# Kernel tuning notes

Hardware: AMD Instinct MI355X
Metric: run time of the kernel (lower is better)

The kernel has to match this reference:

```python
import jax, jax.numpy as jnp
import numpy as np

USER_NUM = 100000
ITEM_NUM = 100000
DIM = 64
BS = 256


def setup_inputs() -> dict:
    key = jax.random.key(0)
    k1, k2, k3, k4, k5 = jax.random.split(key, 5)
    # xavier_normal-ish scale for embeddings/linear
    user_table = jax.random.normal(k1, (USER_NUM, DIM), dtype=jnp.float32) * 0.1
    item_table = jax.random.normal(k2, (ITEM_NUM, DIM), dtype=jnp.float32) * 0.1
    cls_w = jax.random.normal(k3, (5, DIM), dtype=jnp.float32) * (2.0 / (DIM + 5)) ** 0.5
    cls_b = jnp.zeros((5,), dtype=jnp.float32)
    batch_user = jax.random.randint(k4, (BS,), 0, USER_NUM, dtype=jnp.int64)
    values = jnp.array([[1.0, 2.0, 3.0, 4.0, 5.0]], dtype=jnp.float32)
    return {
        "batch_user": batch_user,
        "user_table": user_table,
        "item_table": item_table,
        "cls_w": cls_w,
        "cls_b": cls_b,
        "values": values,
    }


def reference(batch_user, user_table, item_table, cls_w, cls_b, values):
    # forward_full_items: score every (user, item) pair.
    # Torch materializes h_ui = (u repeated) * (items tiled) of shape
    # [bs*item_num, dim]; mathematically logits = einsum over dim, so we
    # fuse the broadcasted product with the tiny Linear to avoid the
    # huge expanded intermediate while computing identical math.
    u = user_table[batch_user]                       # [bs, dim]
    # logits[b,i,c] = sum_d u[b,d] * item[i,d] * W[c,d] + b[c]
    logits = jnp.einsum('bd,id,cd->bic', u, item_table, cls_w) + cls_b  # [bs, item_num, 5]
    prob = jax.nn.softmax(logits, axis=-1)
    return jnp.sum(prob * values[0], axis=-1)        # [bs, item_num]
```

## Files before the change

kernel.cpp:

```cpp
#include <hip/hip_runtime.h>

#define I_TOTAL 100000
#define DIM 64
#define BS 256

typedef __attribute__((ext_vector_type(8))) short bf16x8;
typedef __attribute__((ext_vector_type(4))) float f32x4;

__device__ inline unsigned short f2bf(float x) {
    union { float f; unsigned u; } v; v.f = x;
    return (unsigned short)((v.u + 0x8000u) >> 16);
}

__device__ inline unsigned pk_bf16(float lo, float hi) {
    unsigned r;
    asm("v_cvt_pk_bf16_f32 %0, %1, %2" : "=v"(r) : "v"(lo), "v"(hi));
    return r;
}

__device__ inline bf16x8 pack8(float4 a, float4 b) {
    union { unsigned u[4]; bf16x8 v; } r;
    r.u[0] = pk_bf16(a.x, a.y);
    r.u[1] = pk_bf16(a.z, a.w);
    r.u[2] = pk_bf16(b.x, b.y);
    r.u[3] = pk_bf16(b.z, b.w);
    return r.v;
}

__device__ inline float rfl(float x) {
    union { float f; int i; } u; u.f = x;
    u.i = __builtin_amdgcn_readfirstlane(u.i);
    return u.f;
}

__global__ __launch_bounds__(256) void conv_items(
    const float* __restrict__ item, unsigned short* __restrict__ itbf)
{
    long t = (long)blockIdx.x * 256 + threadIdx.x;
    const float4* p = (const float4*)(item + t * 8);
    float4 a = p[0], b = p[1];
    ushort4 r0, r1;
    r0.x = f2bf(a.x); r0.y = f2bf(a.y); r0.z = f2bf(a.z); r0.w = f2bf(a.w);
    r1.x = f2bf(b.x); r1.y = f2bf(b.y); r1.z = f2bf(b.z); r1.w = f2bf(b.w);
    ushort4* q = (ushort4*)(itbf + t * 8);
    q[0] = r0; q[1] = r1;
}

__device__ inline void mfma_tile(const bf16x8 (&afr)[5][2], bf16x8 b0, bf16x8 b1,
                                 f32x4 (&acc)[5])
{
    const f32x4 zero = (f32x4){0.f, 0.f, 0.f, 0.f};
#pragma unroll
    for (int c = 0; c < 5; ++c) {
        acc[c] = __builtin_amdgcn_mfma_f32_16x16x32_bf16(afr[c][0], b0, zero, 0, 0, 0);
        acc[c] = __builtin_amdgcn_mfma_f32_16x16x32_bf16(afr[c][1], b1, acc[c], 0, 0, 0);
    }
}

__device__ inline void softmax_store(const f32x4 (&acc)[5], const float (&sw)[5],
                                     const float (&swv)[5], float* wlds, int ti)
{
#pragma unroll
    for (int rr = 0; rr < 4; ++rr) {
        float e0 = __builtin_amdgcn_exp2f(acc[0][rr]);
        float e1 = __builtin_amdgcn_exp2f(acc[1][rr]);
        float e2 = __builtin_amdgcn_exp2f(acc[2][rr]);
        float e3 = __builtin_amdgcn_exp2f(acc[3][rr]);
        float e4 = __builtin_amdgcn_exp2f(acc[4][rr]);
        float den = e0 * sw[0];
        den = fmaf(e1, sw[1], den);
        den = fmaf(e2, sw[2], den);
        den = fmaf(e3, sw[3], den);
        den = fmaf(e4, sw[4], den);
        float num = e0 * swv[0];
        num = fmaf(e1, swv[1], num);
        num = fmaf(e2, swv[2], num);
        num = fmaf(e3, swv[3], num);
        num = fmaf(e4, swv[4], num);
        wlds[rr * 64 + ti * 16] = num * __builtin_amdgcn_rcpf(den);
    }
}

__global__ __launch_bounds__(256) void gemm_softmax(
    const unsigned short* __restrict__ itbf,
    const int* __restrict__ bu, const float* __restrict__ ut,
    const float* __restrict__ cw, const float* __restrict__ clsb,
    const float* __restrict__ vals, float* __restrict__ out)
{
    __shared__ float ldsb[4224];

    const int blk = blockIdx.x;
    const int r8 = blk & 7;
    const int qq = blk >> 3;
    const int g  = qq & 15;
    const int a  = qq >> 4;
    const int y  = a * 8 + r8;
    if (y >= 98) return;

    const int lane = threadIdx.x & 63;
    const int wave = threadIdx.x >> 6;
    const int col  = lane & 15;
    const int quad = lane >> 4;

    const int b_base = g * 16;
    const int i_base = y * 1024 + wave * 256;

    const float s = 1.4426950408889634f;

    const float* up = ut + (size_t)bu[b_base + col] * DIM + quad * 8;
    float4 u0 = *(const float4*)(up);
    float4 u1 = *(const float4*)(up + 4);
    float4 u2 = *(const float4*)(up + 32);
    float4 u3 = *(const float4*)(up + 36);
    u0.x *= s; u0.y *= s; u0.z *= s; u0.w *= s;
    u1.x *= s; u1.y *= s; u1.z *= s; u1.w *= s;
    u2.x *= s; u2.y *= s; u2.z *= s; u2.w *= s;
    u3.x *= s; u3.y *= s; u3.z *= s; u3.w *= s;

    bf16x8 afr[5][2];
    float sw[5], swv[5];
#pragma unroll
    for (int c = 0; c < 5; ++c) {
        const float* wp = cw + c * DIM + quad * 8;
        float4 w0 = *(const float4*)(wp);
        float4 w1 = *(const float4*)(wp + 4);
        float4 w2 = *(const float4*)(wp + 32);
        float4 w3 = *(const float4*)(wp + 36);
        float4 m0 = make_float4(u0.x*w0.x, u0.y*w0.y, u0.z*w0.z, u0.w*w0.w);
        float4 m1 = make_float4(u1.x*w1.x, u1.y*w1.y, u1.z*w1.z, u1.w*w1.w);
        float4 m2 = make_float4(u2.x*w2.x, u2.y*w2.y, u2.z*w2.z, u2.w*w2.w);
        float4 m3 = make_float4(u3.x*w3.x, u3.y*w3.y, u3.z*w3.z, u3.w*w3.w);
        afr[c][0] = pack8(m0, m1);
        afr[c][1] = pack8(m2, m3);
        float w = __builtin_amdgcn_exp2f(clsb[c] * s);
        sw[c]  = rfl(w);
        swv[c] = rfl(w * vals[c]);
    }

    if (y < 97) {
        float* wlds = ldsb + wave * 1056 + quad * 264 + col;
        const float* rlds = ldsb + wave * 1056 + quad * 264 + 4 * col;

        float* op[4];
#pragma unroll
        for (int k = 0; k < 4; ++k)
            op[k] = out + (size_t)(b_base + quad * 4 + k) * I_TOTAL + (i_base + 4 * col);

        const unsigned short* bp = itbf + (size_t)(i_base + col) * DIM + quad * 8;

        bf16x8 pf0 = *(const bf16x8*)(bp);
        bf16x8 pf1 = *(const bf16x8*)(bp + 32);

        f32x4 accA[5], accB[5];

#pragma unroll 1
        for (int t4 = 0; t4 < 4; ++t4) {
            const unsigned short* base = bp + (size_t)(t4 * 4) * 1024;
            bf16x8 b0, b1;

            b0 = pf0; b1 = pf1;
            pf0 = *(const bf16x8*)(base + 1024);
            pf1 = *(const bf16x8*)(base + 1024 + 32);
            mfma_tile(afr, b0, b1, accA);

            b0 = pf0; b1 = pf1;
            pf0 = *(const bf16x8*)(base + 2048);
            pf1 = *(const bf16x8*)(base + 2048 + 32);
            mfma_tile(afr, b0, b1, accB);
            softmax_store(accA, sw, swv, wlds, 0);

            b0 = pf0; b1 = pf1;
            pf0 = *(const bf16x8*)(base + 3072);
            pf1 = *(const bf16x8*)(base + 3072 + 32);
            mfma_tile(afr, b0, b1, accA);
            softmax_store(accB, sw, swv, wlds, 1);

            b0 = pf0; b1 = pf1;
            pf0 = *(const bf16x8*)(base + 4096);
            pf1 = *(const bf16x8*)(base + 4096 + 32);
            mfma_tile(afr, b0, b1, accB);
            softmax_store(accA, sw, swv, wlds, 2);

            softmax_store(accB, sw, swv, wlds, 3);

#pragma unroll
            for (int k = 0; k < 4; ++k) {
                f32x4 o4 = *(const f32x4*)(rlds + k * 64);
                *(f32x4*)op[k] = o4;
                op[k] += 64;
            }
        }
    } else {
        float vv[5];
#pragma unroll
        for (int c = 0; c < 5; ++c) vv[c] = vals[c];
#pragma unroll 1
        for (int t = 0; t < 16; ++t) {
            int i  = i_base + t * 16 + col;
            int ic = i < I_TOTAL ? i : I_TOTAL - 1;
            const unsigned short* p2 = itbf + (size_t)ic * DIM + quad * 8;
            bf16x8 b0 = *(const bf16x8*)p2;
            bf16x8 b1 = *(const bf16x8*)(p2 + 32);
            f32x4 acc[5];
            mfma_tile(afr, b0, b1, acc);
            if (i < I_TOTAL) {
#pragma unroll
                for (int rr = 0; rr < 4; ++rr) {
                    float e0 = __builtin_amdgcn_exp2f(acc[0][rr]);
                    float e1 = __builtin_amdgcn_exp2f(acc[1][rr]);
                    float e2 = __builtin_amdgcn_exp2f(acc[2][rr]);
                    float e3 = __builtin_amdgcn_exp2f(acc[3][rr]);
                    float e4 = __builtin_amdgcn_exp2f(acc[4][rr]);
                    float den = e0 * sw[0];
                    den = fmaf(e1, sw[1], den);
                    den = fmaf(e2, sw[2], den);
                    den = fmaf(e3, sw[3], den);
                    den = fmaf(e4, sw[4], den);
                    float num = e0 * swv[0];
                    num = fmaf(e1, swv[1], num);
                    num = fmaf(e2, swv[2], num);
                    num = fmaf(e3, swv[3], num);
                    num = fmaf(e4, swv[4], num);
                    out[(size_t)(b_base + quad * 4 + rr) * I_TOTAL + i] =
                        num * __builtin_amdgcn_rcpf(den);
                }
            }
        }
        (void)vv;
    }
}

__global__ __launch_bounds__(256) void gemm_softmax_fb(
    const int* __restrict__ bu, const float* __restrict__ ut,
    const float* __restrict__ it, const float* __restrict__ cw,
    const float* __restrict__ clsb, const float* __restrict__ vals,
    float* __restrict__ out)
{
    __shared__ float ldsb[4224];

    const int blk = blockIdx.x;
    const int r8 = blk & 7;
    const int qq = blk >> 3;
    const int g  = qq & 15;
    const int a  = qq >> 4;
    const int y  = a * 8 + r8;
    if (y >= 98) return;

    const int lane = threadIdx.x & 63;
    const int wave = threadIdx.x >> 6;
    const int col  = lane & 15;
    const int quad = lane >> 4;

    const int b_base = g * 16;
    const int i_base = y * 1024 + wave * 256;

    const float s = 1.4426950408889634f;

    const float* up = ut + (size_t)bu[b_base + col] * DIM + quad * 8;
    float4 u0 = *(const float4*)(up);
    float4 u1 = *(const float4*)(up + 4);
    float4 u2 = *(const float4*)(up + 32);
    float4 u3 = *(const float4*)(up + 36);
    u0.x *= s; u0.y *= s; u0.z *= s; u0.w *= s;
    u1.x *= s; u1.y *= s; u1.z *= s; u1.w *= s;
    u2.x *= s; u2.y *= s; u2.z *= s; u2.w *= s;
    u3.x *= s; u3.y *= s; u3.z *= s; u3.w *= s;

    bf16x8 afr[5][2];
    f32x4 cin[5];
    float vv[5];
#pragma unroll
    for (int c = 0; c < 5; ++c) {
        const float* wp = cw + c * DIM + quad * 8;
        float4 w0 = *(const float4*)(wp);
        float4 w1 = *(const float4*)(wp + 4);
        float4 w2 = *(const float4*)(wp + 32);
        float4 w3 = *(const float4*)(wp + 36);
        float4 m0 = make_float4(u0.x*w0.x, u0.y*w0.y, u0.z*w0.z, u0.w*w0.w);
        float4 m1 = make_float4(u1.x*w1.x, u1.y*w1.y, u1.z*w1.z, u1.w*w1.w);
        float4 m2 = make_float4(u2.x*w2.x, u2.y*w2.y, u2.z*w2.z, u2.w*w2.w);
        float4 m3 = make_float4(u3.x*w3.x, u3.y*w3.y, u3.z*w3.z, u3.w*w3.w);
        afr[c][0] = pack8(m0, m1);
        afr[c][1] = pack8(m2, m3);
        float bc = clsb[c] * s;
        cin[c] = (f32x4){bc, bc, bc, bc};
        vv[c] = vals[c];
    }

    if (y < 97) {
        float* wlds = ldsb + wave * 1056 + quad * 264 + col;
        const float* rlds = ldsb + wave * 1056 + quad * 264 + 4 * col;

        float* op[4];
#pragma unroll
        for (int k = 0; k < 4; ++k)
            op[k] = out + (size_t)(b_base + quad * 4 + k) * I_TOTAL + (i_base + 4 * col);

        const float* bp = it + (size_t)(i_base + col) * DIM + quad * 8;

#pragma unroll 1
        for (int t4 = 0; t4 < 4; ++t4) {
#pragma unroll
            for (int ti = 0; ti < 4; ++ti) {
                const float* p = bp + ti * 1024;
                float4 q0 = *(const float4*)(p);
                float4 q1 = *(const float4*)(p + 4);
                float4 q2 = *(const float4*)(p + 32);
                float4 q3 = *(const float4*)(p + 36);
                bf16x8 b0 = pack8(q0, q1);
                bf16x8 b1 = pack8(q2, q3);
                f32x4 acc[5];
#pragma unroll
                for (int c = 0; c < 5; ++c) {
                    acc[c] = __builtin_amdgcn_mfma_f32_16x16x32_bf16(afr[c][0], b0, cin[c], 0, 0, 0);
                    acc[c] = __builtin_amdgcn_mfma_f32_16x16x32_bf16(afr[c][1], b1, acc[c], 0, 0, 0);
                }
#pragma unroll
                for (int rr = 0; rr < 4; ++rr) {
                    float e0 = __builtin_amdgcn_exp2f(acc[0][rr]);
                    float e1 = __builtin_amdgcn_exp2f(acc[1][rr]);
                    float e2 = __builtin_amdgcn_exp2f(acc[2][rr]);
                    float e3 = __builtin_amdgcn_exp2f(acc[3][rr]);
                    float e4 = __builtin_amdgcn_exp2f(acc[4][rr]);
                    float den = ((e0 + e1) + (e2 + e3)) + e4;
                    float num = e0 * vv[0];
                    num = fmaf(e1, vv[1], num);
                    num = fmaf(e2, vv[2], num);
                    num = fmaf(e3, vv[3], num);
                    num = fmaf(e4, vv[4], num);
                    wlds[rr * 64 + ti * 16] = num * __builtin_amdgcn_rcpf(den);
                }
            }
#pragma unroll
            for (int k = 0; k < 4; ++k) {
                f32x4 o4 = *(const f32x4*)(rlds + k * 64);
                *(f32x4*)op[k] = o4;
                op[k] += 64;
            }
            bp += 4 * 1024;
        }
    } else {
#pragma unroll 1
        for (int t = 0; t < 16; ++t) {
            int i  = i_base + t * 16 + col;
            int ic = i < I_TOTAL ? i : I_TOTAL - 1;
            const float* p2 = it + (size_t)ic * DIM + quad * 8;
            float4 q0 = *(const float4*)(p2);
            float4 q1 = *(const float4*)(p2 + 4);
            float4 q2 = *(const float4*)(p2 + 32);
            float4 q3 = *(const float4*)(p2 + 36);
            bf16x8 b0 = pack8(q0, q1);
            bf16x8 b1 = pack8(q2, q3);
            f32x4 acc[5];
#pragma unroll
            for (int c = 0; c < 5; ++c) {
                acc[c] = __builtin_amdgcn_mfma_f32_16x16x32_bf16(afr[c][0], b0, cin[c], 0, 0, 0);
                acc[c] = __builtin_amdgcn_mfma_f32_16x16x32_bf16(afr[c][1], b1, acc[c], 0, 0, 0);
            }
            if (i < I_TOTAL) {
#pragma unroll
                for (int rr = 0; rr < 4; ++rr) {
                    float e0 = __builtin_amdgcn_exp2f(acc[0][rr]);
                    float e1 = __builtin_amdgcn_exp2f(acc[1][rr]);
                    float e2 = __builtin_amdgcn_exp2f(acc[2][rr]);
                    float e3 = __builtin_amdgcn_exp2f(acc[3][rr]);
                    float e4 = __builtin_amdgcn_exp2f(acc[4][rr]);
                    float den = ((e0 + e1) + (e2 + e3)) + e4;
                    float num = e0 * vv[0];
                    num = fmaf(e1, vv[1], num);
                    num = fmaf(e2, vv[2], num);
                    num = fmaf(e3, vv[3], num);
                    num = fmaf(e4, vv[4], num);
                    out[(size_t)(b_base + quad * 4 + rr) * I_TOTAL + i] =
                        num * __builtin_amdgcn_rcpf(den);
                }
            }
        }
    }
}

extern "C" void kernel_launch(void* const* d_in, const int* in_sizes, int n_in,
                              void* d_out, int out_size, void* d_ws, size_t ws_size,
                              hipStream_t stream) {
    const int*   bu   = (const int*)d_in[0];
    const float* ut   = (const float*)d_in[1];
    const float* it   = (const float*)d_in[2];
    const float* cw   = (const float*)d_in[3];
    const float* cb   = (const float*)d_in[4];
    const float* vals = (const float*)d_in[5];
    float* out = (float*)d_out;
    unsigned short* itbf = (unsigned short*)d_ws;

    const size_t needed = (size_t)I_TOTAL * DIM * 2;

    if (ws_size >= needed) {
        conv_items<<<3125, 256, 0, stream>>>(it, itbf);
        gemm_softmax<<<1664, 256, 0, stream>>>(itbf, bu, ut, cw, cb, vals, out);
    } else {
        gemm_softmax_fb<<<1664, 256, 0, stream>>>(bu, ut, it, cw, cb, vals, out);
    }
}
```

Before: 177.8 us.

## Split fused GEMM-softmax blocks into single-wave workgroups and drop manual prefetch

The main kernel now launches one wave per workgroup (6656 blocks of 64 threads) instead of four waves per block, with the wave index folded into the block index and a smaller LDS buffer per block. The hand-written software prefetch and double accumulator pipeline is replaced by a simple unrolled loop over four tiles, leaving scheduling to the compiler. The fallback kernel is refactored to use the shared mfma_tile/softmax_store helpers with the exp-bias weighting. The smaller blocks aim to improve scheduling granularity and occupancy, but they lose the explicit load/compute overlap.

```diff
diff --git a/kernel.cpp b/kernel.cpp
--- a/kernel.cpp
+++ b/kernel.cpp
@@ -81,29 +81,30 @@
     }
 }
 
-__global__ __launch_bounds__(256) void gemm_softmax(
+__global__ __launch_bounds__(64) void gemm_softmax(
     const unsigned short* __restrict__ itbf,
     const int* __restrict__ bu, const float* __restrict__ ut,
     const float* __restrict__ cw, const float* __restrict__ clsb,
     const float* __restrict__ vals, float* __restrict__ out)
 {
-    __shared__ float ldsb[4224];
-
-    const int blk = blockIdx.x;
-    const int r8 = blk & 7;
-    const int qq = blk >> 3;
-    const int g  = qq & 15;
-    const int a  = qq >> 4;
-    const int y  = a * 8 + r8;
+    __shared__ float ldsb[1056];
+
+    const int blk  = blockIdx.x;
+    const int r8   = blk & 7;
+    const int rest = blk >> 3;
+    const int wv   = rest & 3;
+    const int qq   = rest >> 2;
+    const int g    = qq & 15;
+    const int a    = qq >> 4;
+    const int y    = a * 8 + r8;
     if (y >= 98) return;
 
     const int lane = threadIdx.x & 63;
-    const int wave = threadIdx.x >> 6;
     const int col  = lane & 15;
     const int quad = lane >> 4;
 
     const int b_base = g * 16;
-    const int i_base = y * 1024 + wave * 256;
+    const int i_base = y * 1024 + wv * 256;
 
     const float s = 1.4426950408889634f;
 
@@ -138,8 +139,8 @@
     }
 
     if (y < 97) {
-        float* wlds = ldsb + wave * 1056 + quad * 264 + col;
-        const float* rlds = ldsb + wave * 1056 + quad * 264 + 4 * col;
+        float* wlds = ldsb + quad * 264 + col;
+        const float* rlds = ldsb + quad * 264 + 4 * col;
 
         float* op[4];
 #pragma unroll
@@ -148,52 +149,25 @@
 
         const unsigned short* bp = itbf + (size_t)(i_base + col) * DIM + quad * 8;
 
-        bf16x8 pf0 = *(const bf16x8*)(bp);
-        bf16x8 pf1 = *(const bf16x8*)(bp + 32);
-
-        f32x4 accA[5], accB[5];
-
 #pragma unroll 1
         for (int t4 = 0; t4 < 4; ++t4) {
-            const unsigned short* base = bp + (size_t)(t4 * 4) * 1024;
-            bf16x8 b0, b1;
-
-            b0 = pf0; b1 = pf1;
-            pf0 = *(const bf16x8*)(base + 1024);
-            pf1 = *(const bf16x8*)(base + 1024 + 32);
-            mfma_tile(afr, b0, b1, accA);
-
-            b0 = pf0; b1 = pf1;
-            pf0 = *(const bf16x8*)(base + 2048);
-            pf1 = *(const bf16x8*)(base + 2048 + 32);
-            mfma_tile(afr, b0, b1, accB);
-            softmax_store(accA, sw, swv, wlds, 0);
-
-            b0 = pf0; b1 = pf1;
-            pf0 = *(const bf16x8*)(base + 3072);
-            pf1 = *(const bf16x8*)(base + 3072 + 32);
-            mfma_tile(afr, b0, b1, accA);
-            softmax_store(accB, sw, swv, wlds, 1);
-
-            b0 = pf0; b1 = pf1;
-            pf0 = *(const bf16x8*)(base + 4096);
-            pf1 = *(const bf16x8*)(base + 4096 + 32);
-            mfma_tile(afr, b0, b1, accB);
-            softmax_store(accA, sw, swv, wlds, 2);
-
-            softmax_store(accB, sw, swv, wlds, 3);
-
+#pragma unroll
+            for (int ti = 0; ti < 4; ++ti) {
+                bf16x8 b0 = *(const bf16x8*)(bp + ti * 1024);
+                bf16x8 b1 = *(const bf16x8*)(bp + ti * 1024 + 32);
+                f32x4 acc[5];
+                mfma_tile(afr, b0, b1, acc);
+                softmax_store(acc, sw, swv, wlds, ti);
+            }
 #pragma unroll
             for (int k = 0; k < 4; ++k) {
                 f32x4 o4 = *(const f32x4*)(rlds + k * 64);
                 *(f32x4*)op[k] = o4;
                 op[k] += 64;
             }
+            bp += 4 * 1024;
         }
     } else {
-        float vv[5];
-#pragma unroll
-        for (int c = 0; c < 5; ++c) vv[c] = vals[c];
 #pragma unroll 1
         for (int t = 0; t < 16; ++t) {
             int i  = i_base + t * 16 + col;
@@ -226,7 +200,6 @@
                 }
             }
         }
-        (void)vv;
     }
 }
 
@@ -267,8 +240,7 @@
     u3.x *= s; u3.y *= s; u3.z *= s; u3.w *= s;
 
     bf16x8 afr[5][2];
-    f32x4 cin[5];
-    float vv[5];
+    float sw[5], swv[5];
 #pragma unroll
     for (int c = 0; c < 5; ++c) {
         const float* wp = cw + c * DIM + quad * 8;
@@ -282,9 +254,9 @@
         float4 m3 = make_float4(u3.x*w3.x, u3.y*w3.y, u3.z*w3.z, u3.w*w3.w);
         afr[c][0] = pack8(m0, m1);
         afr[c][1] = pack8(m2, m3);
-        float bc = clsb[c] * s;
-        cin[c] = (f32x4){bc, bc, bc, bc};
-        vv[c] = vals[c];
+        float w = __builtin_amdgcn_exp2f(clsb[c] * s);
+        sw[c]  = rfl(w);
+        swv[c] = rfl(w * vals[c]);
     }
 
     if (y < 97) {
@@ -310,26 +282,8 @@
                 bf16x8 b0 = pack8(q0, q1);
                 bf16x8 b1 = pack8(q2, q3);
                 f32x4 acc[5];
-#pragma unroll
-                for (int c = 0; c < 5; ++c) {
-                    acc[c] = __builtin_amdgcn_mfma_f32_16x16x32_bf16(afr[c][0], b0, cin[c], 0, 0, 0);
-                    acc[c] = __builtin_amdgcn_mfma_f32_16x16x32_bf16(afr[c][1], b1, acc[c], 0, 0, 0);
-                }
-#pragma unroll
-                for (int rr = 0; rr < 4; ++rr) {
-                    float e0 = __builtin_amdgcn_exp2f(acc[0][rr]);
-                    float e1 = __builtin_amdgcn_exp2f(acc[1][rr]);
-                    float e2 = __builtin_amdgcn_exp2f(acc[2][rr]);
-                    float e3 = __builtin_amdgcn_exp2f(acc[3][rr]);
-                    float e4 = __builtin_amdgcn_exp2f(acc[4][rr]);
-                    float den = ((e0 + e1) + (e2 + e3)) + e4;
-                    float num = e0 * vv[0];
-                    num = fmaf(e1, vv[1], num);
-                    num = fmaf(e2, vv[2], num);
-                    num = fmaf(e3, vv[3], num);
-                    num = fmaf(e4, vv[4], num);
-                    wlds[rr * 64 + ti * 16] = num * __builtin_amdgcn_rcpf(den);
-                }
+                mfma_tile(afr, b0, b1, acc);
+                softmax_store(acc, sw, swv, wlds, ti);
             }
 #pragma unroll
             for (int k = 0; k < 4; ++k) {
@@ -352,11 +306,7 @@
             bf16x8 b0 = pack8(q0, q1);
             bf16x8 b1 = pack8(q2, q3);
             f32x4 acc[5];
-#pragma unroll
-            for (int c = 0; c < 5; ++c) {
-                acc[c] = __builtin_amdgcn_mfma_f32_16x16x32_bf16(afr[c][0], b0, cin[c], 0, 0, 0);
-                acc[c] = __builtin_amdgcn_mfma_f32_16x16x32_bf16(afr[c][1], b1, acc[c], 0, 0, 0);
-            }
+            mfma_tile(afr, b0, b1, acc);
             if (i < I_TOTAL) {
 #pragma unroll
                 for (int rr = 0; rr < 4; ++rr) {
@@ -365,12 +315,16 @@
                     float e2 = __builtin_amdgcn_exp2f(acc[2][rr]);
                     float e3 = __builtin_amdgcn_exp2f(acc[3][rr]);
                     float e4 = __builtin_amdgcn_exp2f(acc[4][rr]);
-                    float den = ((e0 + e1) + (e2 + e3)) + e4;
-                    float num = e0 * vv[0];
-                    num = fmaf(e1, vv[1], num);
-                    num = fmaf(e2, vv[2], num);
-                    num = fmaf(e3, vv[3], num);
-                    num = fmaf(e4, vv[4], num);
+                    float den = e0 * sw[0];
+                    den = fmaf(e1, sw[1], den);
+                    den = fmaf(e2, sw[2], den);
+                    den = fmaf(e3, sw[3], den);
+                    den = fmaf(e4, sw[4], den);
+                    float num = e0 * swv[0];
+                    num = fmaf(e1, swv[1], num);
+                    num = fmaf(e2, swv[2], num);
+                    num = fmaf(e3, swv[3], num);
+                    num = fmaf(e4, swv[4], num);
                     out[(size_t)(b_base + quad * 4 + rr) * I_TOTAL + i] =
                         num * __builtin_amdgcn_rcpf(den);
                 }
@@ -395,7 +349,7 @@
 
     if (ws_size >= needed) {
         conv_items<<<3125, 256, 0, stream>>>(it, itbf);
-        gemm_softmax<<<1664, 256, 0, stream>>>(itbf, bu, ut, cw, cb, vals, out);
+        gemm_softmax<<<6656, 64, 0, stream>>>(itbf, bu, ut, cw, cb, vals, out);
     } else {
         gemm_softmax_fb<<<1664, 256, 0, stream>>>(bu, ut, it, cw, cb, vals, out);
     }
```

Measured after the change: 174.6 us. Within noise of the previous version (-1.8%).
